# Kernel optimization log

Measured on AMD Instinct MI355X. Metric: run time of the kernel, lower is better.

## Reference

```python
import jax, jax.numpy as jnp
import numpy as np

EMBED_DIM = 64
NUM_ITEM = 1000000
BATCH = 131072
SEQ_LEN = 5
# fixed_arc = "AND,0,~1;OR,2,3;AND,5,6;OR,~7,4" parsed: (module, (pos, negated), (pos, negated))
ARC = [("AND", (0, False), (1, True)),
       ("OR",  (2, False), (3, False)),
       ("AND", (5, False), (6, False)),
       ("OR",  (7, True),  (4, False))]


def setup_inputs() -> dict:
    key = jax.random.key(0)
    ks = jax.random.split(key, 20)
    std = 0.01  # init_params: normal(0, 0.01)
    inp = {}
    inp["seq"] = jax.random.randint(ks[0], (BATCH, SEQ_LEN), 0, NUM_ITEM, dtype=jnp.int32)
    inp["pos_target"] = jax.random.randint(ks[1], (BATCH,), 0, NUM_ITEM, dtype=jnp.int32)
    inp["neg_target"] = jax.random.randint(ks[2], (BATCH,), 0, NUM_ITEM, dtype=jnp.int32)
    inp["item_embed"] = std * jax.random.normal(ks[3], (NUM_ITEM, EMBED_DIM), dtype=jnp.float32)
    t = jax.random.uniform(ks[4], (EMBED_DIM,), minval=0.0, maxval=0.1, dtype=jnp.float32)
    inp["true_vec"] = t / jnp.maximum(jnp.linalg.norm(t), 1e-12)
    inp["not_W1"] = std * jax.random.normal(ks[5], (EMBED_DIM, EMBED_DIM), dtype=jnp.float32)
    inp["not_b1"] = std * jax.random.normal(ks[6], (EMBED_DIM,), dtype=jnp.float32)
    inp["not_W2"] = std * jax.random.normal(ks[7], (EMBED_DIM, EMBED_DIM), dtype=jnp.float32)
    inp["not_b2"] = std * jax.random.normal(ks[8], (EMBED_DIM,), dtype=jnp.float32)
    inp["and_W1"] = std * jax.random.normal(ks[9], (2 * EMBED_DIM, EMBED_DIM), dtype=jnp.float32)
    inp["and_b1"] = std * jax.random.normal(ks[10], (EMBED_DIM,), dtype=jnp.float32)
    inp["and_W2"] = std * jax.random.normal(ks[11], (EMBED_DIM, EMBED_DIM), dtype=jnp.float32)
    inp["and_b2"] = std * jax.random.normal(ks[12], (EMBED_DIM,), dtype=jnp.float32)
    inp["or_W1"] = std * jax.random.normal(ks[13], (2 * EMBED_DIM, EMBED_DIM), dtype=jnp.float32)
    inp["or_b1"] = std * jax.random.normal(ks[14], (EMBED_DIM,), dtype=jnp.float32)
    inp["or_W2"] = std * jax.random.normal(ks[15], (EMBED_DIM, EMBED_DIM), dtype=jnp.float32)
    inp["or_b2"] = std * jax.random.normal(ks[16], (EMBED_DIM,), dtype=jnp.float32)
    return inp


def _mlp(x, W1, b1, W2, b2):
    # _get_ln_module(num_layers=2, dropout=0): Linear -> LeakyReLU -> Dropout(0) -> Linear
    h = jax.nn.leaky_relu(x @ W1 + b1, negative_slope=0.01)
    return h @ W2 + b2


def reference(seq, pos_target, neg_target, item_embed, true_vec,
              not_W1, not_b1, not_W2, not_b2,
              and_W1, and_b1, and_W2, and_b2,
              or_W1, or_b1, or_W2, or_b2):
    NOT = lambda x: _mlp(x, not_W1, not_b1, not_W2, not_b2)
    AND = lambda x: _mlp(x, and_W1, and_b1, and_W2, and_b2)
    OR = lambda x: _mlp(x, or_W1, or_b1, or_W2, or_b2)
    mods = {"AND": AND, "OR": OR}

    intermediates = {}

    def get_input(pos, neg):
        if pos < SEQ_LEN:
            e = item_embed[seq[:, pos]]  # [B, D] embedding gather
        else:
            e = intermediates[pos]
        return NOT(e) if neg else e

    out = None
    for layer_id, (name, (p1, n1), (p2, n2)) in enumerate(ARC):
        i1 = get_input(p1, n1)
        i2 = get_input(p2, n2)
        out = mods[name](jnp.concatenate((i1, i2), axis=-1))
        intermediates[SEQ_LEN + layer_id] = out

    enc_not = NOT(out)  # [B, D]
    pos_e = item_embed[pos_target]
    neg_e = item_embed[neg_target]
    encoded_pos = OR(jnp.concatenate((enc_not, pos_e), axis=-1))
    encoded_neg = OR(jnp.concatenate((enc_not, neg_e), axis=-1))
    encoded = jnp.concatenate((encoded_pos, encoded_neg), axis=0)  # [2B, D]

    # cosine similarity vs 'true' anchor, amplified by 10 (cos_amplify_factor)
    eps = 1e-8
    num = encoded @ true_vec
    denom = jnp.maximum(jnp.linalg.norm(encoded, axis=-1), eps) * jnp.maximum(jnp.linalg.norm(true_vec), eps)
    prediction = (num / denom) * 10.0
    return prediction
```

## Files before the change

### kernel.cpp

```cpp
#include <hip/hip_runtime.h>
#include <stdint.h>
#include <math.h>

#define BATCH 131072
#define WS_TN_OFF 65536
#define WS_B_OFF  65544

typedef __attribute__((ext_vector_type(8)))  short short8;
typedef __attribute__((ext_vector_type(16))) float float16;
typedef __attribute__((ext_vector_type(2)))  unsigned int uint2v;

union S8 { short8 s; uint32_t u[4]; };
union F8 { float f[8]; uint32_t u[8]; float4 v4[2]; };

__global__ __launch_bounds__(256)
void prep_kernel(const float* __restrict__ tvec,
                 const float* __restrict__ nW1, const float* __restrict__ nW2,
                 const float* __restrict__ aW1, const float* __restrict__ aW2,
                 const float* __restrict__ oW1, const float* __restrict__ oW2,
                 const float* __restrict__ nb1, const float* __restrict__ nb2,
                 const float* __restrict__ ab1, const float* __restrict__ ab2,
                 const float* __restrict__ ob1, const float* __restrict__ ob2,
                 char* __restrict__ ws)
{
    const int id = blockIdx.x * 256 + threadIdx.x;
    if (id == 0) {
        float s = 0.f;
        for (int j = 0; j < 64; ++j) s = fmaf(tvec[j], tvec[j], s);
        *(float*)(ws + WS_TN_OFF) = fmaxf(sqrtf(s), 1e-8f);
    }
    if (id < 32768) {
        const float* srcs[8] = { nW1, nW2, aW1, aW1 + 4096, aW2, oW1, oW1 + 4096, oW2 };
        const int u    = id >> 12;
        const int e    = id & 4095;
        const int j    = e & 7;
        const int lane = (e >> 3) & 63;
        const int f    = e >> 9;
        const int nt   = f & 1, kc = f >> 1;
        const int k    = kc * 16 + (lane >> 5) * 8 + j;
        const int n    = nt * 32 + (lane & 31);
        const uint32_t b = __float_as_uint(srcs[u][k * 64 + n]);
        const uint32_t r = b + 0x7fffu + ((b >> 16) & 1u);
        ((uint16_t*)(ws + u * 8192 + f * 1024 + lane * 16))[j] = (uint16_t)(r >> 16);
    } else if (id < 33152) {
        const int b   = id - 32768;
        const int arr = b >> 6, j = b & 63;
        const float* bp = (arr == 0) ? nb1 : (arr == 1) ? nb2 : (arr == 2) ? ab1
                        : (arr == 3) ? ab2 : (arr == 4) ? ob1 : ob2;
        ((float*)(ws + WS_B_OFF))[b] = bp[j];
    } else if (id < 33216) {
        const int j = id - 33152;
        ((float*)(ws + WS_B_OFF + 1536))[j] = tvec[j];
    }
}

#define OPW(g,u,sH,ini,bid,ep,rd,sl) \
    ((g)|((u)<<3)|((sH)<<6)|((ini)<<7)|((bid)<<8)|((ep)<<11)|((rd)<<13)|((sl)<<15))

__global__ __launch_bounds__(256, 3)
void logicnet_mfma(const int* __restrict__ seq, const int* __restrict__ post,
                   const int* __restrict__ negt, const float* __restrict__ E,
                   const char* __restrict__ ws, float* __restrict__ out)
{
    static const uint32_t PROG[24] = {
        OPW(3,5,0,1,4,0,0,0),
        OPW(4,6,0,0,0,1,0,0),
        OPW(0,7,0,1,5,3,0,0),
        OPW(2,0,0,1,0,1,0,0),
        OPW(0,1,0,1,1,2,0,0),
        OPW(0,3,0,1,2,0,0,0),
        OPW(1,2,0,0,0,1,0,0),
        OPW(0,4,0,1,3,2,0,0),
        OPW(0,2,0,1,2,0,0,0),
        OPW(0,3,1,0,0,1,0,0),
        OPW(0,4,0,1,3,2,0,0),
        OPW(0,0,0,1,0,1,0,0),
        OPW(0,1,0,1,1,2,0,0),
        OPW(0,5,0,1,4,0,0,0),
        OPW(5,6,0,0,0,1,0,0),
        OPW(0,7,0,1,5,2,0,0),
        OPW(0,0,0,1,0,1,0,0),
        OPW(0,1,0,1,1,3,0,1),
        OPW(0,5,1,1,4,0,0,1),
        OPW(6,6,0,0,0,1,0,0),
        OPW(0,7,0,1,5,0,1,0),
        OPW(0,5,1,1,4,0,0,1),
        OPW(7,6,0,0,0,1,0,0),
        OPW(0,7,0,1,5,0,2,0),
    };

    __shared__ float lds[448];
    const int tid  = threadIdx.x;
    const int wid  = tid >> 6;
    const int lane = tid & 63;
    const int m    = lane & 31;
    const int h    = lane >> 5;
    const int rowbase = (blockIdx.x * 4 + wid) * 32;
    const int rr   = rowbase + m;

    for (int t = tid; t < 448; t += 256) lds[t] = ((const float*)(ws + WS_B_OFF))[t];
    __syncthreads();
    const float* const ldsb = lds;
    const float* const ltv  = lds + 384;

    const float tn = *(const float*)(ws + WS_TN_OFF);

    const int sv0 = seq[(size_t)rr * 5 + 0], sv1 = seq[(size_t)rr * 5 + 1];
    const int sv2 = seq[(size_t)rr * 5 + 2], sv3 = seq[(size_t)rr * 5 + 3];
    const int sv4 = seq[(size_t)rr * 5 + 4];
    const int ipv = post[rr], imv = negt[rr];

    float16 acc[2];
    S8 xhi[4], xlo[4];
    S8 i6f[4], encf[4];

    auto gw = [&](int idx) {
        const float4* e = (const float4*)(E + (size_t)idx * 64 + h * 8);
        F8 x[4];
#pragma unroll
        for (int kc = 0; kc < 4; ++kc) { x[kc].v4[0] = e[kc * 4]; x[kc].v4[1] = e[kc * 4 + 1]; }
#pragma unroll
        for (int kc = 0; kc < 4; ++kc) {
#pragma unroll
            for (int w = 0; w < 4; ++w) {
                const uint32_t b0 = x[kc].u[2 * w], b1 = x[kc].u[2 * w + 1];
                xhi[kc].u[w] = __builtin_amdgcn_perm(b1, b0, 0x07060302u);
                const float l0 = x[kc].f[2 * w]     - __uint_as_float(b0 & 0xffff0000u);
                const float l1 = x[kc].f[2 * w + 1] - __uint_as_float(b1 & 0xffff0000u);
                xlo[kc].u[w] = __builtin_amdgcn_perm(__float_as_uint(l1), __float_as_uint(l0), 0x07060302u);
            }
        }
    };

    auto uaP = [&](int u) {
        const char* wb = ws + u * 8192 + lane * 16;
#pragma unroll
        for (int kc = 0; kc < 4; ++kc) {
            const short8 w0 = *(const short8*)(wb + (kc * 2 + 0) * 1024);
            const short8 w1 = *(const short8*)(wb + (kc * 2 + 1) * 1024);
            acc[0] = __builtin_amdgcn_mfma_f32_32x32x16_bf16(w0, xhi[kc].s, acc[0], 0, 0, 0);
            acc[1] = __builtin_amdgcn_mfma_f32_32x32x16_bf16(w1, xhi[kc].s, acc[1], 0, 0, 0);
            acc[0] = __builtin_amdgcn_mfma_f32_32x32x16_bf16(w0, xlo[kc].s, acc[0], 0, 0, 0);
            acc[1] = __builtin_amdgcn_mfma_f32_32x32x16_bf16(w1, xlo[kc].s, acc[1], 0, 0, 0);
        }
    };

    auto uaH = [&](int u, const S8* xf) {
        const char* wb = ws + u * 8192 + lane * 16;
#pragma unroll
        for (int kc = 0; kc < 4; ++kc) {
            const short8 w0 = *(const short8*)(wb + (kc * 2 + 0) * 1024);
            const short8 w1 = *(const short8*)(wb + (kc * 2 + 1) * 1024);
            acc[0] = __builtin_amdgcn_mfma_f32_32x32x16_bf16(w0, xf[kc].s, acc[0], 0, 0, 0);
            acc[1] = __builtin_amdgcn_mfma_f32_32x32x16_bf16(w1, xf[kc].s, acc[1], 0, 0, 0);
        }
    };

    auto epiX = [&](bool act) {
#pragma unroll
        for (int nt = 0; nt < 2; ++nt) {
#pragma unroll
            for (int c = 0; c < 2; ++c) {
                uint32_t ph[2][2], pl[2][2];
#pragma unroll
                for (int d = 0; d < 2; ++d) {
                    const int g2 = 2 * c + d;
                    float v0 = acc[nt][4 * g2 + 0], v1 = acc[nt][4 * g2 + 1];
                    float v2 = acc[nt][4 * g2 + 2], v3 = acc[nt][4 * g2 + 3];
                    if (act) {
                        v0 = fmaxf(v0, 0.01f * v0); v1 = fmaxf(v1, 0.01f * v1);
                        v2 = fmaxf(v2, 0.01f * v2); v3 = fmaxf(v3, 0.01f * v3);
                    }
                    const uint32_t b0 = __float_as_uint(v0), b1 = __float_as_uint(v1);
                    const uint32_t b2 = __float_as_uint(v2), b3 = __float_as_uint(v3);
                    ph[d][0] = __builtin_amdgcn_perm(b1, b0, 0x07060302u);
                    ph[d][1] = __builtin_amdgcn_perm(b3, b2, 0x07060302u);
                    const float l0 = v0 - __uint_as_float(b0 & 0xffff0000u);
                    const float l1 = v1 - __uint_as_float(b1 & 0xffff0000u);
                    const float l2 = v2 - __uint_as_float(b2 & 0xffff0000u);
                    const float l3 = v3 - __uint_as_float(b3 & 0xffff0000u);
                    pl[d][0] = __builtin_amdgcn_perm(__float_as_uint(l1), __float_as_uint(l0), 0x07060302u);
                    pl[d][1] = __builtin_amdgcn_perm(__float_as_uint(l3), __float_as_uint(l2), 0x07060302u);
                }
                const int kc = 2 * nt + c;
#pragma unroll
                for (int w = 0; w < 2; ++w) {
                    uint2v rh = __builtin_amdgcn_permlane32_swap(ph[0][w], ph[1][w], false, false);
                    xhi[kc].u[w]     = rh[0];
                    xhi[kc].u[2 + w] = rh[1];
                    uint2v rl = __builtin_amdgcn_permlane32_swap(pl[0][w], pl[1][w], false, false);
                    xlo[kc].u[w]     = rl[0];
                    xlo[kc].u[2 + w] = rl[1];
                }
            }
        }
    };

    auto epiB = [&](S8* dst) {
#pragma unroll
        for (int nt = 0; nt < 2; ++nt) {
#pragma unroll
            for (int c = 0; c < 2; ++c) {
                uint32_t pp[2][2];
#pragma unroll
                for (int d = 0; d < 2; ++d) {
                    const int g2 = 2 * c + d;
                    asm("v_cvt_pk_bf16_f32 %0, %1, %2"
                        : "=v"(pp[d][0]) : "v"(acc[nt][4 * g2 + 0]), "v"(acc[nt][4 * g2 + 1]));
                    asm("v_cvt_pk_bf16_f32 %0, %1, %2"
                        : "=v"(pp[d][1]) : "v"(acc[nt][4 * g2 + 2]), "v"(acc[nt][4 * g2 + 3]));
                }
                const int kc = 2 * nt + c;
#pragma unroll
                for (int w = 0; w < 2; ++w) {
                    uint2v r = __builtin_amdgcn_permlane32_swap(pp[0][w], pp[1][w], false, false);
                    dst[kc].u[w]     = r[0];
                    dst[kc].u[2 + w] = r[1];
                }
            }
        }
    };

    auto reduce = [&](float* outp) {
        float num = 0.f, ss = 0.f;
#pragma unroll
        for (int nt = 0; nt < 2; ++nt)
#pragma unroll
            for (int g2 = 0; g2 < 4; ++g2) {
                const float4 t4 = *(const float4*)(ltv + nt * 32 + g2 * 8 + h * 4);
                const float y0 = acc[nt][4 * g2 + 0], y1 = acc[nt][4 * g2 + 1];
                const float y2 = acc[nt][4 * g2 + 2], y3 = acc[nt][4 * g2 + 3];
                num = fmaf(y0, t4.x, fmaf(y1, t4.y, fmaf(y2, t4.z, fmaf(y3, t4.w, num))));
                ss  = fmaf(y0, y0, fmaf(y1, y1, fmaf(y2, y2, fmaf(y3, y3, ss))));
            }
        num += __shfl_xor(num, 32, 64);
        ss  += __shfl_xor(ss, 32, 64);
        if (h == 0) outp[m] = num / (fmaxf(sqrtf(ss), 1e-8f) * tn) * 10.0f;
    };

#pragma unroll 1
    for (int op = 0; op < 24; ++op) {
        const uint32_t cw = PROG[op];
        const int g   = cw & 7;
        const int u   = (cw >> 3) & 7;
        const int sH  = (cw >> 6) & 1;
        const int ini = (cw >> 7) & 1;
        const int bid = (cw >> 8) & 7;
        const int ep  = (cw >> 11) & 3;
        const int rd  = (cw >> 13) & 3;
        const int sl  = (cw >> 15) & 1;

        if (g) {
            int idx;
            switch (g) {
                case 1: idx = sv0; break;
                case 2: idx = sv1; break;
                case 3: idx = sv2; break;
                case 4: idx = sv3; break;
                case 5: idx = sv4; break;
                case 6: idx = ipv; break;
                default: idx = imv; break;
            }
            gw(idx);
        }
        if (ini) {
#pragma unroll
            for (int nt = 0; nt < 2; ++nt)
#pragma unroll
                for (int g2 = 0; g2 < 4; ++g2) {
                    const float4 b4 = *(const float4*)(ldsb + bid * 64 + nt * 32 + g2 * 8 + h * 4);
                    acc[nt][4 * g2 + 0] = b4.x; acc[nt][4 * g2 + 1] = b4.y;
                    acc[nt][4 * g2 + 2] = b4.z; acc[nt][4 * g2 + 3] = b4.w;
                }
        }
        if (sH) { if (sl) uaH(u, encf); else uaH(u, i6f); }
        else    uaP(u);

        if (ep == 1)      epiX(true);
        else if (ep == 2) epiX(false);
        else if (ep == 3) { if (sl) epiB(encf); else epiB(i6f); }

        if (rd == 1)      reduce(out + rowbase);
        else if (rd == 2) reduce(out + BATCH + rowbase);
    }
}

extern "C" void kernel_launch(void* const* d_in, const int* in_sizes, int n_in,
                              void* d_out, int out_size, void* d_ws, size_t ws_size,
                              hipStream_t stream) {
    const int*   seq  = (const int*)  d_in[0];
    const int*   post = (const int*)  d_in[1];
    const int*   negt = (const int*)  d_in[2];
    const float* E    = (const float*)d_in[3];
    const float* tv   = (const float*)d_in[4];
    const float* nW1  = (const float*)d_in[5];
    const float* nb1  = (const float*)d_in[6];
    const float* nW2  = (const float*)d_in[7];
    const float* nb2  = (const float*)d_in[8];
    const float* aW1  = (const float*)d_in[9];
    const float* ab1  = (const float*)d_in[10];
    const float* aW2  = (const float*)d_in[11];
    const float* ab2  = (const float*)d_in[12];
    const float* oW1  = (const float*)d_in[13];
    const float* ob1  = (const float*)d_in[14];
    const float* oW2  = (const float*)d_in[15];
    const float* ob2  = (const float*)d_in[16];
    float* out = (float*)d_out;
    char*  ws  = (char*)d_ws;

    hipLaunchKernelGGL(prep_kernel, dim3(130), dim3(256), 0, stream,
                       tv, nW1, nW2, aW1, aW2, oW1, oW2,
                       nb1, nb2, ab1, ab2, ob1, ob2, ws);
    hipLaunchKernelGGL(logicnet_mfma, dim3(BATCH / 128), dim3(256), 0, stream,
                       seq, post, negt, E, ws, out);
}
```

Measured before the change: 440.8 us.

## Prefetch embedding gathers one op ahead and spill saved fragments to LDS

Splits each embedding gather into an issue step and a later pack step. Loads for the next needed row are issued right after the current op's MFMAs, so gather latency overlaps the epilogue and the following op. The saved bf16 fragments (i6f, encf) move from registers into swizzled per-wave LDS slots, which frees VGPRs so launch bounds can rise from 3 to 4 waves occupancy. MFMA sections get raised priority via s_setprio. The cost is extra LDS traffic and 32KB of LDS per block, which could itself limit occupancy.

```diff
diff --git a/kernel.cpp b/kernel.cpp
--- a/kernel.cpp
+++ b/kernel.cpp
@@ -54,42 +54,42 @@
     }
 }
 
-#define OPW(g,u,sH,ini,bid,ep,rd,sl) \
-    ((g)|((u)<<3)|((sH)<<6)|((ini)<<7)|((bid)<<8)|((ep)<<11)|((rd)<<13)|((sl)<<15))
-
-__global__ __launch_bounds__(256, 3)
+#define OPW(g,u,sH,ini,bid,ep,rd,sl,pg,alt) \
+    ((g)|((u)<<3)|((sH)<<6)|((ini)<<7)|((bid)<<8)|((ep)<<11)|((rd)<<13)|((sl)<<15)|((pg)<<16)|((alt)<<19))
+
+__global__ __launch_bounds__(256, 4)
 void logicnet_mfma(const int* __restrict__ seq, const int* __restrict__ post,
                    const int* __restrict__ negt, const float* __restrict__ E,
                    const char* __restrict__ ws, float* __restrict__ out)
 {
     static const uint32_t PROG[24] = {
-        OPW(3,5,0,1,4,0,0,0),
-        OPW(4,6,0,0,0,1,0,0),
-        OPW(0,7,0,1,5,3,0,0),
-        OPW(2,0,0,1,0,1,0,0),
-        OPW(0,1,0,1,1,2,0,0),
-        OPW(0,3,0,1,2,0,0,0),
-        OPW(1,2,0,0,0,1,0,0),
-        OPW(0,4,0,1,3,2,0,0),
-        OPW(0,2,0,1,2,0,0,0),
-        OPW(0,3,1,0,0,1,0,0),
-        OPW(0,4,0,1,3,2,0,0),
-        OPW(0,0,0,1,0,1,0,0),
-        OPW(0,1,0,1,1,2,0,0),
-        OPW(0,5,0,1,4,0,0,0),
-        OPW(5,6,0,0,0,1,0,0),
-        OPW(0,7,0,1,5,2,0,0),
-        OPW(0,0,0,1,0,1,0,0),
-        OPW(0,1,0,1,1,3,0,1),
-        OPW(0,5,1,1,4,0,0,1),
-        OPW(6,6,0,0,0,1,0,0),
-        OPW(0,7,0,1,5,0,1,0),
-        OPW(0,5,1,1,4,0,0,1),
-        OPW(7,6,0,0,0,1,0,0),
-        OPW(0,7,0,1,5,0,2,0),
-    };
-
-    __shared__ float lds[448];
+        OPW(0,5,0,1,4,0,0,0,0,0),
+        OPW(4,6,0,0,0,1,0,0,2,1),
+        OPW(0,7,0,1,5,3,0,0,0,0),
+        OPW(2,0,0,1,0,1,0,0,1,0),
+        OPW(0,1,0,1,1,2,0,0,0,0),
+        OPW(0,3,0,1,2,0,0,0,0,0),
+        OPW(1,2,0,0,0,1,0,0,0,0),
+        OPW(0,4,0,1,3,2,0,0,0,0),
+        OPW(0,2,0,1,2,0,0,0,0,0),
+        OPW(0,3,1,0,0,1,0,0,0,0),
+        OPW(0,4,0,1,3,2,0,0,0,0),
+        OPW(0,0,0,1,0,1,0,0,5,0),
+        OPW(0,1,0,1,1,2,0,0,0,0),
+        OPW(0,5,0,1,4,0,0,0,0,0),
+        OPW(5,6,0,0,0,1,0,0,0,0),
+        OPW(0,7,0,1,5,2,0,0,0,0),
+        OPW(0,0,0,1,0,1,0,0,6,0),
+        OPW(0,1,0,1,1,3,0,1,0,0),
+        OPW(0,5,1,1,4,0,0,1,0,0),
+        OPW(6,6,0,0,0,1,0,0,7,0),
+        OPW(0,7,0,1,5,0,1,0,0,0),
+        OPW(0,5,1,1,4,0,0,1,0,0),
+        OPW(7,6,0,0,0,1,0,0,0,0),
+        OPW(0,7,0,1,5,0,2,0,0,0),
+    };
+
+    __shared__ uint32_t lds[448 + 4096 + 4096];
     const int tid  = threadIdx.x;
     const int wid  = tid >> 6;
     const int lane = tid & 63;
@@ -98,12 +98,10 @@
     const int rowbase = (blockIdx.x * 4 + wid) * 32;
     const int rr   = rowbase + m;
 
-    for (int t = tid; t < 448; t += 256) lds[t] = ((const float*)(ws + WS_B_OFF))[t];
-    __syncthreads();
-    const float* const ldsb = lds;
-    const float* const ltv  = lds + 384;
-
-    const float tn = *(const float*)(ws + WS_TN_OFF);
+    uint32_t* const slot0 = &lds[448 + wid * 1024];
+    uint32_t* const slot1 = &lds[448 + 4096 + wid * 1024];
+    const float* const ldsb = (const float*)lds;
+    const float* const ltv  = (const float*)(lds + 384);
 
     const int sv0 = seq[(size_t)rr * 5 + 0], sv1 = seq[(size_t)rr * 5 + 1];
     const int sv2 = seq[(size_t)rr * 5 + 2], sv3 = seq[(size_t)rr * 5 + 3];
@@ -112,21 +110,23 @@
 
     float16 acc[2];
     S8 xhi[4], xlo[4];
-    S8 i6f[4], encf[4];
-
-    auto gw = [&](int idx) {
+    F8 gx[4], gx2[4];
+    float tn;
+
+    auto gissue = [&](F8* dst, int idx) {
         const float4* e = (const float4*)(E + (size_t)idx * 64 + h * 8);
-        F8 x[4];
-#pragma unroll
-        for (int kc = 0; kc < 4; ++kc) { x[kc].v4[0] = e[kc * 4]; x[kc].v4[1] = e[kc * 4 + 1]; }
+#pragma unroll
+        for (int kc = 0; kc < 4; ++kc) { dst[kc].v4[0] = e[kc * 4]; dst[kc].v4[1] = e[kc * 4 + 1]; }
+    };
+    auto gpack = [&](const F8* src) {
 #pragma unroll
         for (int kc = 0; kc < 4; ++kc) {
 #pragma unroll
             for (int w = 0; w < 4; ++w) {
-                const uint32_t b0 = x[kc].u[2 * w], b1 = x[kc].u[2 * w + 1];
+                const uint32_t b0 = src[kc].u[2 * w], b1 = src[kc].u[2 * w + 1];
                 xhi[kc].u[w] = __builtin_amdgcn_perm(b1, b0, 0x07060302u);
-                const float l0 = x[kc].f[2 * w]     - __uint_as_float(b0 & 0xffff0000u);
-                const float l1 = x[kc].f[2 * w + 1] - __uint_as_float(b1 & 0xffff0000u);
+                const float l0 = src[kc].f[2 * w]     - __uint_as_float(b0 & 0xffff0000u);
+                const float l1 = src[kc].f[2 * w + 1] - __uint_as_float(b1 & 0xffff0000u);
                 xlo[kc].u[w] = __builtin_amdgcn_perm(__float_as_uint(l1), __float_as_uint(l0), 0x07060302u);
             }
         }
@@ -145,14 +145,15 @@
         }
     };
 
-    auto uaH = [&](int u, const S8* xf) {
+    auto uaH = [&](int u, const uint32_t* slot) {
         const char* wb = ws + u * 8192 + lane * 16;
 #pragma unroll
         for (int kc = 0; kc < 4; ++kc) {
+            const short8 xf = *(const short8*)(slot + lane * 16 + ((kc ^ (lane & 3)) << 2));
             const short8 w0 = *(const short8*)(wb + (kc * 2 + 0) * 1024);
             const short8 w1 = *(const short8*)(wb + (kc * 2 + 1) * 1024);
-            acc[0] = __builtin_amdgcn_mfma_f32_32x32x16_bf16(w0, xf[kc].s, acc[0], 0, 0, 0);
-            acc[1] = __builtin_amdgcn_mfma_f32_32x32x16_bf16(w1, xf[kc].s, acc[1], 0, 0, 0);
+            acc[0] = __builtin_amdgcn_mfma_f32_32x32x16_bf16(w0, xf, acc[0], 0, 0, 0);
+            acc[1] = __builtin_amdgcn_mfma_f32_32x32x16_bf16(w1, xf, acc[1], 0, 0, 0);
         }
     };
 
@@ -196,7 +197,7 @@
         }
     };
 
-    auto epiB = [&](S8* dst) {
+    auto epiB = [&](uint32_t* slot) {
 #pragma unroll
         for (int nt = 0; nt < 2; ++nt) {
 #pragma unroll
@@ -211,12 +212,14 @@
                         : "=v"(pp[d][1]) : "v"(acc[nt][4 * g2 + 2]), "v"(acc[nt][4 * g2 + 3]));
                 }
                 const int kc = 2 * nt + c;
+                S8 o;
 #pragma unroll
                 for (int w = 0; w < 2; ++w) {
                     uint2v r = __builtin_amdgcn_permlane32_swap(pp[0][w], pp[1][w], false, false);
-                    dst[kc].u[w]     = r[0];
-                    dst[kc].u[2 + w] = r[1];
-                }
+                    o.u[w]     = r[0];
+                    o.u[2 + w] = r[1];
+                }
+                *(short8*)(slot + lane * 16 + ((kc ^ (lane & 3)) << 2)) = o.s;
             }
         }
     };
@@ -237,6 +240,13 @@
         ss  += __shfl_xor(ss, 32, 64);
         if (h == 0) outp[m] = num / (fmaxf(sqrtf(ss), 1e-8f) * tn) * 10.0f;
     };
+
+    for (int t = tid; t < 448; t += 256) lds[t] = ((const uint32_t*)(ws + WS_B_OFF))[t];
+    gissue(gx,  sv2);
+    gissue(gx2, sv3);
+    gpack(gx);
+    __syncthreads();
+    tn = *(const float*)(ws + WS_TN_OFF);
 
 #pragma unroll 1
     for (int op = 0; op < 24; ++op) {
@@ -249,10 +259,30 @@
         const int ep  = (cw >> 11) & 3;
         const int rd  = (cw >> 13) & 3;
         const int sl  = (cw >> 15) & 1;
-
-        if (g) {
+        const int pg  = (cw >> 16) & 7;
+        const int alt = (cw >> 19) & 1;
+
+        if (g) gpack(alt ? gx2 : gx);
+
+        if (ini) {
+#pragma unroll
+            for (int nt = 0; nt < 2; ++nt)
+#pragma unroll
+                for (int g2 = 0; g2 < 4; ++g2) {
+                    const float4 b4 = *(const float4*)(ldsb + bid * 64 + nt * 32 + g2 * 8 + h * 4);
+                    acc[nt][4 * g2 + 0] = b4.x; acc[nt][4 * g2 + 1] = b4.y;
+                    acc[nt][4 * g2 + 2] = b4.z; acc[nt][4 * g2 + 3] = b4.w;
+                }
+        }
+
+        __builtin_amdgcn_s_setprio(1);
+        if (sH) uaH(u, sl ? slot1 : slot0);
+        else    uaP(u);
+        __builtin_amdgcn_s_setprio(0);
+
+        if (pg) {
             int idx;
-            switch (g) {
+            switch (pg) {
                 case 1: idx = sv0; break;
                 case 2: idx = sv1; break;
                 case 3: idx = sv2; break;
@@ -261,24 +291,12 @@
                 case 6: idx = ipv; break;
                 default: idx = imv; break;
             }
-            gw(idx);
-        }
-        if (ini) {
-#pragma unroll
-            for (int nt = 0; nt < 2; ++nt)
-#pragma unroll
-                for (int g2 = 0; g2 < 4; ++g2) {
-                    const float4 b4 = *(const float4*)(ldsb + bid * 64 + nt * 32 + g2 * 8 + h * 4);
-                    acc[nt][4 * g2 + 0] = b4.x; acc[nt][4 * g2 + 1] = b4.y;
-                    acc[nt][4 * g2 + 2] = b4.z; acc[nt][4 * g2 + 3] = b4.w;
-                }
-        }
-        if (sH) { if (sl) uaH(u, encf); else uaH(u, i6f); }
-        else    uaP(u);
+            gissue(gx, idx);
+        }
 
         if (ep == 1)      epiX(true);
         else if (ep == 2) epiX(false);
-        else if (ep == 3) { if (sl) epiB(encf); else epiB(i6f); }
+        else if (ep == 3) epiB(sl ? slot1 : slot0);
 
         if (rd == 1)      reduce(out + rowbase);
         else if (rd == 2) reduce(out + BATCH + rowbase);
```

Result: slower. 582.9 us (+32.2%).
